# Optimization experiments

Measured on AMD Instinct MI355X. Metric: run time of the kernel, lower is better.

The kernel has to match this reference:

```python
import jax, jax.numpy as jnp
import numpy as np


def setup_inputs() -> dict:
    key = jax.random.key(0)
    k1, k2 = jax.random.split(key)
    B, S, D, E = 8, 8192, 512, 209
    x = jax.random.normal(k1, (B, S, D), dtype=jnp.float32)
    # nn.init.normal_(std=0.01)
    gate_w = jax.random.normal(k2, (E, D), dtype=jnp.float32) * 0.01
    expert_counts = jnp.zeros((E,), dtype=jnp.float32)
    gate_probs_sum = jnp.zeros((E,), dtype=jnp.float32)
    return {"x": x, "gate_w": gate_w, "expert_counts": expert_counts,
            "gate_probs_sum": gate_probs_sum}


def reference(x, gate_w, expert_counts, gate_probs_sum):
    B, S, D = x.shape
    E = gate_w.shape[0]
    x_flat = x.reshape(-1, D)                      # [N, D]
    n_tokens = x_flat.shape[0]
    gate_logits = jnp.einsum('nd,ed->ne', x_flat, gate_w)   # [N, E]
    gate_probs = jax.nn.softmax(gate_logits, axis=-1)
    gate_scores = jnp.max(gate_probs, axis=-1)               # [N]
    expert_indices = jnp.argmax(gate_probs, axis=-1)         # [N] int
    # one-hot sum over tokens == histogram of expert assignments
    tokens_per_expert_actual = jnp.zeros((E,), dtype=jnp.float32).at[expert_indices].add(1.0)
    gate_mean = jnp.mean(gate_probs, axis=0)                 # [E]
    load_balancing_loss = E * jnp.sum(gate_mean * tokens_per_expert_actual) / n_tokens
    # EMA buffer updates (no-grad in the original)
    new_expert_counts = 0.9 * expert_counts + 0.1 * tokens_per_expert_actual
    new_gate_probs_sum = 0.9 * gate_probs_sum + 0.1 * jnp.sum(gate_probs, axis=0)
    return (x_flat, gate_scores, expert_indices, load_balancing_loss,
            new_expert_counts, new_gate_probs_sum)
```

## Files before the change

kernel.cpp:

```cpp
#include <hip/hip_runtime.h>

#define DK 512
#define NSTEP 16
#define NPANEL 14
#define EPAD 224
#define LP 225
#define WFRAG_ELEMS (EPAD * DK)
#define STEPB 14336

typedef __attribute__((ext_vector_type(8))) short bf16x8;
typedef __attribute__((ext_vector_type(4))) float f32x4;

__device__ __forceinline__ unsigned short f2b(float f) {
    unsigned u = __float_as_uint(f);
    return (unsigned short)((u + 0x7fffu + ((u >> 16) & 1u)) >> 16);
}
__device__ __forceinline__ float b2f(unsigned short h) {
    return __uint_as_float((unsigned)h << 16);
}
__device__ __forceinline__ void split4(float4 v, ushort4& h, ushort4& lo) {
    h.x = f2b(v.x); h.y = f2b(v.y); h.z = f2b(v.z); h.w = f2b(v.w);
    lo.x = f2b(v.x - b2f(h.x)); lo.y = f2b(v.y - b2f(h.y));
    lo.z = f2b(v.z - b2f(h.z)); lo.w = f2b(v.w - b2f(h.w));
}
__device__ __forceinline__ void pack8(float4 a, float4 b, bf16x8& h, bf16x8& lo) {
    float v[8] = {a.x, a.y, a.z, a.w, b.x, b.y, b.z, b.w};
    #pragma unroll
    for (int j = 0; j < 8; ++j) {
        unsigned u = __float_as_uint(v[j]);
        h[j]  = (short)(u >> 16);
        lo[j] = (short)f2b(v[j] - __uint_as_float(u & 0xffff0000u));
    }
}
__device__ __forceinline__ void gld16(const void* g, void* l) {
    __builtin_amdgcn_global_load_lds(
        (const __attribute__((address_space(1))) unsigned int*)g,
        (__attribute__((address_space(3))) unsigned int*)l, 16, 0, 0);
}

extern "C" __global__ void moe_init(float* hist, float* probsum, int* cnt) {
    int t = threadIdx.x;
    if (t < EPAD) { hist[t] = 0.f; probsum[t] = 0.f; }
    if (t == 0) *cnt = 0;
}

extern "C" __global__ void __launch_bounds__(256)
moe_prep(const float* __restrict__ w,
         unsigned short* __restrict__ wHi,
         unsigned short* __restrict__ wLo, int E)
{
    int g = blockIdx.x * 256 + threadIdx.x;
    int l  = g & 63;
    int pc = g >> 6;
    int kk = pc / NPANEL;
    int p  = pc - kk * NPANEL;
    int e  = p * 16 + (l & 15);
    int k0 = kk * 32 + (l >> 4) * 8;
    float4 v0 = make_float4(0.f,0.f,0.f,0.f), v1 = v0;
    if (e < E) {
        v0 = *(const float4*)(w + (size_t)e * DK + k0);
        v1 = *(const float4*)(w + (size_t)e * DK + k0 + 4);
    }
    ushort4 h0, l0, h1, l1;
    split4(v0, h0, l0); split4(v1, h1, l1);
    size_t off = (size_t)g * 8;
    *(ushort4*)(wHi + off)     = h0;
    *(ushort4*)(wHi + off + 4) = h1;
    *(ushort4*)(wLo + off)     = l0;
    *(ushort4*)(wLo + off + 4) = l1;
}

extern "C" __global__ void __launch_bounds__(256, 2)
moe_gemm(const float* __restrict__ x,
         const unsigned short* __restrict__ wHi,
         const unsigned short* __restrict__ wLo,
         float* __restrict__ out,
         float* __restrict__ hist,
         float* __restrict__ probsum_g,
         int* __restrict__ flag_cnt,
         int* __restrict__ flag_list,
         int flag_cap, int N, int E)
{
    __shared__ char Bl[2][2 * STEPB];
    __shared__ float ps_l[EPAD];
    __shared__ float tok_m[32], tok_s[32];

    const int t    = threadIdx.x;
    const int l    = t & 63;
    const int wid  = t >> 6;
    const int wm   = wid >> 1;
    const int wn   = wid & 1;
    const int le   = l & 15;
    const int lg   = l >> 4;
    const int tok0 = blockIdx.x * 64;

    if (t < EPAD) ps_l[t] = 0.f;

    f32x4 acc[2][7];
    #pragma unroll
    for (int mi = 0; mi < 2; ++mi)
        #pragma unroll
        for (int j = 0; j < 7; ++j)
            acc[mi][j] = (f32x4){0.f, 0.f, 0.f, 0.f};

    #define STAGE_B(kk_, buf_)                                                  \
        {   _Pragma("unroll")                                                   \
            for (int i_ = 0; i_ < 7; ++i_) {                                    \
                int c_ = wid * 7 + i_;                                          \
                const char* src_ = (c_ < NPANEL)                                \
                    ? ((const char*)wHi + (kk_) * STEPB + c_ * 1024 + l * 16)   \
                    : ((const char*)wLo + (kk_) * STEPB + (c_ - NPANEL) * 1024 + l * 16); \
                gld16(src_, (buf_) + c_ * 1024);                                \
            }                                                                   \
        }

    float4 Areg[2][2][2];
    #pragma unroll
    for (int mi = 0; mi < 2; ++mi) {
        const float* ar = x + (size_t)(tok0 + wm * 32 + mi * 16 + le) * DK + lg * 8;
        Areg[0][mi][0] = *(const float4*)(ar);
        Areg[0][mi][1] = *(const float4*)(ar + 4);
    }
    STAGE_B(0, Bl[0]);
    __syncthreads();

    #pragma unroll
    for (int kk = 0; kk < NSTEP; ++kk) {
        const int p = kk & 1;
        if (kk + 1 < NSTEP) {
            #pragma unroll
            for (int mi = 0; mi < 2; ++mi) {
                const float* ar = x + (size_t)(tok0 + wm * 32 + mi * 16 + le) * DK
                                + (kk + 1) * 32 + lg * 8;
                Areg[1 - p][mi][0] = *(const float4*)(ar);
                Areg[1 - p][mi][1] = *(const float4*)(ar + 4);
            }
            STAGE_B(kk + 1, Bl[1 - p]);
        }
        if (wn == 0) {
            #pragma unroll
            for (int mi = 0; mi < 2; ++mi) {
                float* ow = out + (size_t)(tok0 + wm * 32 + mi * 16 + le) * DK
                          + kk * 32 + lg * 8;
                *(float4*)ow       = Areg[p][mi][0];
                *(float4*)(ow + 4) = Areg[p][mi][1];
            }
        }
        bf16x8 ah[2], al[2];
        pack8(Areg[p][0][0], Areg[p][0][1], ah[0], al[0]);
        pack8(Areg[p][1][0], Areg[p][1][1], ah[1], al[1]);
        #pragma unroll
        for (int j = 0; j < 7; ++j) {
            int q = wn * 7 + j;
            bf16x8 bh = *(const bf16x8*)(&Bl[p][q * 1024 + l * 16]);
            bf16x8 bl = *(const bf16x8*)(&Bl[p][STEPB + q * 1024 + l * 16]);
            #pragma unroll
            for (int mi = 0; mi < 2; ++mi) {
                acc[mi][j] = __builtin_amdgcn_mfma_f32_16x16x32_bf16(ah[mi], bh, acc[mi][j], 0, 0, 0);
                acc[mi][j] = __builtin_amdgcn_mfma_f32_16x16x32_bf16(ah[mi], bl, acc[mi][j], 0, 0, 0);
                acc[mi][j] = __builtin_amdgcn_mfma_f32_16x16x32_bf16(al[mi], bh, acc[mi][j], 0, 0, 0);
            }
        }
        __syncthreads();
    }

    float* logits = (float*)&Bl[0][0];

    for (int pass = 0; pass < 2; ++pass) {
        __syncthreads();
        if (wm == pass) {
            #pragma unroll
            for (int mi = 0; mi < 2; ++mi)
                #pragma unroll
                for (int nj = 0; nj < 7; ++nj)
                    #pragma unroll
                    for (int rg = 0; rg < 4; ++rg) {
                        int rr = mi * 16 + (l >> 4) * 4 + rg;
                        int cc = wn * 112 + nj * 16 + (l & 15);
                        logits[rr * LP + cc] = acc[mi][nj][rg];
                    }
        }
        __syncthreads();
        {
            int r = t >> 3, sub = t & 7;
            float m1 = -1e30f, m2 = -1e30f;
            int i1 = 0x7fffffff;
            for (int e = sub; e < E; e += 8) {
                float v = logits[r * LP + e];
                if (v > m1) { m2 = m1; m1 = v; i1 = e; }
                else if (v > m2) { m2 = v; }
            }
            #pragma unroll
            for (int mask = 1; mask < 8; mask <<= 1) {
                float om1 = __shfl_xor(m1, mask);
                float om2 = __shfl_xor(m2, mask);
                int   oi1 = __shfl_xor(i1, mask);
                if (om1 > m1 || (om1 == m1 && oi1 < i1)) {
                    m2 = fmaxf(m1, om2); m1 = om1; i1 = oi1;
                } else {
                    m2 = fmaxf(m2, om1);
                }
            }
            float s = 0.f;
            for (int e = sub; e < E; e += 8) s += __expf(logits[r * LP + e] - m1);
            #pragma unroll
            for (int mask = 1; mask < 8; mask <<= 1) s += __shfl_xor(s, mask);

            if (sub == 0) {
                float sinv = 1.0f / s;
                tok_m[r] = m1; tok_s[r] = sinv;
                int tok = tok0 + pass * 32 + r;
                out[(size_t)N * DK + tok]     = sinv;
                out[(size_t)N * DK + N + tok] = (float)i1;
                atomicAdd(&hist[i1], 1.0f);
                if (m1 - m2 < 2e-4f) {
                    int pos = atomicAdd(flag_cnt, 1);
                    if (pos < flag_cap) flag_list[pos] = tok;
                }
            }
        }
        __syncthreads();
        if (t < E) {
            float sum = 0.f;
            #pragma unroll 4
            for (int r = 0; r < 32; ++r)
                sum += __expf(logits[r * LP + t] - tok_m[r]) * tok_s[r];
            ps_l[t] += sum;
        }
    }
    __syncthreads();
    if (t < E) atomicAdd(&probsum_g[t], ps_l[t]);
    #undef STAGE_B
}

extern "C" __global__ void __launch_bounds__(256)
moe_refine(const float* __restrict__ x,
           const float* __restrict__ w,
           float* __restrict__ hist,
           const int* __restrict__ flag_cnt,
           const int* __restrict__ flag_list,
           int flag_cap,
           float* __restrict__ out,
           int N, int E)
{
    __shared__ float  xsh[DK];
    __shared__ double rv[256];
    __shared__ int    ri[256];
    int nf = *flag_cnt; if (nf > flag_cap) nf = flag_cap;
    const int tid = threadIdx.x;

    for (int li = blockIdx.x; li < nf; li += gridDim.x) {
        int tok = flag_list[li];
        for (int k = tid; k < DK; k += 256) xsh[k] = x[(size_t)tok * DK + k];
        __syncthreads();
        double a = -1e300;
        if (tid < E) {
            const float* wr = w + (size_t)tid * DK;
            double a0 = 0, a1 = 0, a2 = 0, a3 = 0;
            for (int k = 0; k < DK; k += 4) {
                a0 += (double)xsh[k]     * (double)wr[k];
                a1 += (double)xsh[k + 1] * (double)wr[k + 1];
                a2 += (double)xsh[k + 2] * (double)wr[k + 2];
                a3 += (double)xsh[k + 3] * (double)wr[k + 3];
            }
            a = (a0 + a1) + (a2 + a3);
        }
        rv[tid] = a; ri[tid] = tid;
        __syncthreads();
        for (int s = 128; s > 0; s >>= 1) {
            if (tid < s) {
                double vb = rv[tid + s]; int ib = ri[tid + s];
                double va = rv[tid];     int ia = ri[tid];
                if (vb > va || (vb == va && ib < ia)) { rv[tid] = vb; ri[tid] = ib; }
            }
            __syncthreads();
        }
        if (tid == 0) {
            int newi = ri[0];
            int oldi = (int)out[(size_t)N * DK + N + tok];
            if (newi != oldi) {
                atomicAdd(&hist[oldi], -1.0f);
                atomicAdd(&hist[newi],  1.0f);
                out[(size_t)N * DK + N + tok] = (float)newi;
            }
        }
        __syncthreads();
    }
}

extern "C" __global__ void __launch_bounds__(256)
moe_final(const float* __restrict__ hist,
          const float* __restrict__ probsum,
          const float* __restrict__ ec_in,
          const float* __restrict__ gps_in,
          float* __restrict__ out,
          int N, int E)
{
    __shared__ double red[256];
    int t = threadIdx.x;
    double p = 0.0;
    if (t < E) p = (double)hist[t] * (double)probsum[t];
    red[t] = p;
    __syncthreads();
    for (int s = 128; s > 0; s >>= 1) {
        if (t < s) red[t] += red[t + s];
        __syncthreads();
    }
    size_t base = (size_t)N * DK + 2 * (size_t)N;
    if (t == 0) {
        double loss = (double)E * red[0] / ((double)N * (double)N);
        out[base] = (float)loss;
    }
    if (t < E) {
        out[base + 1 + t]     = 0.9f * ec_in[t]  + 0.1f * hist[t];
        out[base + 1 + E + t] = 0.9f * gps_in[t] + 0.1f * probsum[t];
    }
}

extern "C" void kernel_launch(void* const* d_in, const int* in_sizes, int n_in,
                              void* d_out, int out_size, void* d_ws, size_t ws_size,
                              hipStream_t stream)
{
    const float* x   = (const float*)d_in[0];
    const float* w   = (const float*)d_in[1];
    const float* ec  = (const float*)d_in[2];
    const float* gps = (const float*)d_in[3];
    float* out = (float*)d_out;

    int E = in_sizes[2];
    int N = in_sizes[0] / DK;

    unsigned short* wHi = (unsigned short*)d_ws;
    unsigned short* wLo = wHi + WFRAG_ELEMS;
    float* hist    = (float*)(wLo + WFRAG_ELEMS);
    float* probsum = hist + EPAD;
    int*   cnt     = (int*)(probsum + EPAD);
    int*   list    = cnt + 1;
    long long used = 2LL * WFRAG_ELEMS * 2 + 4LL * (2 * EPAD + 1);
    long long cap_ll = ((long long)ws_size - used) / 4;
    int cap = cap_ll < 0 ? 0 : (cap_ll > 65536 ? 65536 : (int)cap_ll);

    moe_prep  <<<56,     256, 0, stream>>>(w, wHi, wLo, E);
    moe_init  <<<1,      256, 0, stream>>>(hist, probsum, cnt);
    moe_gemm  <<<N / 64, 256, 0, stream>>>(x, wHi, wLo, out, hist, probsum, cnt, list, cap, N, E);
    moe_refine<<<256,    256, 0, stream>>>(x, w, hist, cnt, list, cap, out, N, E);
    moe_final <<<1,      256, 0, stream>>>(hist, probsum, ec, gps, out, N, E);
}
```

Measured before the change: 201.0 us.

## Switch gate GEMM to single fp16 MFMA, split x copy into separate kernel

```diff
diff --git a/kernel.cpp b/kernel.cpp
--- a/kernel.cpp
+++ b/kernel.cpp
@@ -5,33 +5,12 @@
 #define NPANEL 14
 #define EPAD 224
 #define LP 225
-#define WFRAG_ELEMS (EPAD * DK)
+#define WF_ELEMS (EPAD * DK)
 #define STEPB 14336
 
-typedef __attribute__((ext_vector_type(8))) short bf16x8;
+typedef __attribute__((ext_vector_type(8))) _Float16 f16x8;
 typedef __attribute__((ext_vector_type(4))) float f32x4;
 
-__device__ __forceinline__ unsigned short f2b(float f) {
-    unsigned u = __float_as_uint(f);
-    return (unsigned short)((u + 0x7fffu + ((u >> 16) & 1u)) >> 16);
-}
-__device__ __forceinline__ float b2f(unsigned short h) {
-    return __uint_as_float((unsigned)h << 16);
-}
-__device__ __forceinline__ void split4(float4 v, ushort4& h, ushort4& lo) {
-    h.x = f2b(v.x); h.y = f2b(v.y); h.z = f2b(v.z); h.w = f2b(v.w);
-    lo.x = f2b(v.x - b2f(h.x)); lo.y = f2b(v.y - b2f(h.y));
-    lo.z = f2b(v.z - b2f(h.z)); lo.w = f2b(v.w - b2f(h.w));
-}
-__device__ __forceinline__ void pack8(float4 a, float4 b, bf16x8& h, bf16x8& lo) {
-    float v[8] = {a.x, a.y, a.z, a.w, b.x, b.y, b.z, b.w};
-    #pragma unroll
-    for (int j = 0; j < 8; ++j) {
-        unsigned u = __float_as_uint(v[j]);
-        h[j]  = (short)(u >> 16);
-        lo[j] = (short)f2b(v[j] - __uint_as_float(u & 0xffff0000u));
-    }
-}
 __device__ __forceinline__ void gld16(const void* g, void* l) {
     __builtin_amdgcn_global_load_lds(
         (const __attribute__((address_space(1))) unsigned int*)g,
@@ -45,9 +24,7 @@
 }
 
 extern "C" __global__ void __launch_bounds__(256)
-moe_prep(const float* __restrict__ w,
-         unsigned short* __restrict__ wHi,
-         unsigned short* __restrict__ wLo, int E)
+moe_prep(const float* __restrict__ w, _Float16* __restrict__ wF, int E)
 {
     int g = blockIdx.x * 256 + threadIdx.x;
     int l  = g & 63;
@@ -61,19 +38,25 @@
         v0 = *(const float4*)(w + (size_t)e * DK + k0);
         v1 = *(const float4*)(w + (size_t)e * DK + k0 + 4);
     }
-    ushort4 h0, l0, h1, l1;
-    split4(v0, h0, l0); split4(v1, h1, l1);
-    size_t off = (size_t)g * 8;
-    *(ushort4*)(wHi + off)     = h0;
-    *(ushort4*)(wHi + off + 4) = h1;
-    *(ushort4*)(wLo + off)     = l0;
-    *(ushort4*)(wLo + off + 4) = l1;
-}
-
-extern "C" __global__ void __launch_bounds__(256, 2)
+    f16x8 h;
+    h[0] = (_Float16)v0.x; h[1] = (_Float16)v0.y;
+    h[2] = (_Float16)v0.z; h[3] = (_Float16)v0.w;
+    h[4] = (_Float16)v1.x; h[5] = (_Float16)v1.y;
+    h[6] = (_Float16)v1.z; h[7] = (_Float16)v1.w;
+    *(f16x8*)(wF + (size_t)g * 8) = h;
+}
+
+extern "C" __global__ void __launch_bounds__(256)
+moe_copy(const float4* __restrict__ xin, float4* __restrict__ outv, int n4)
+{
+    int i = blockIdx.x * 256 + threadIdx.x;
+    int stride = gridDim.x * 256;
+    for (; i < n4; i += stride) outv[i] = xin[i];
+}
+
+extern "C" __global__ void __launch_bounds__(256, 4)
 moe_gemm(const float* __restrict__ x,
-         const unsigned short* __restrict__ wHi,
-         const unsigned short* __restrict__ wLo,
+         const _Float16* __restrict__ wF,
          float* __restrict__ out,
          float* __restrict__ hist,
          float* __restrict__ probsum_g,
@@ -81,9 +64,11 @@
          int* __restrict__ flag_list,
          int flag_cap, int N, int E)
 {
-    __shared__ char Bl[2][2 * STEPB];
+    __shared__ float sbuf[32 * LP];
     __shared__ float ps_l[EPAD];
     __shared__ float tok_m[32], tok_s[32];
+    char* Bl0 = (char*)sbuf;
+    char* Bl1 = (char*)sbuf + STEPB;
 
     const int t    = threadIdx.x;
     const int l    = t & 63;
@@ -93,6 +78,7 @@
     const int le   = l & 15;
     const int lg   = l >> 4;
     const int tok0 = blockIdx.x * 64;
+    const char* wFb = (const char*)wF;
 
     if (t < EPAD) ps_l[t] = 0.f;
 
@@ -103,68 +89,72 @@
         for (int j = 0; j < 7; ++j)
             acc[mi][j] = (f32x4){0.f, 0.f, 0.f, 0.f};
 
+    float4 A0[2][2], A1[2][2];
+
     #define STAGE_B(kk_, buf_)                                                  \
         {   _Pragma("unroll")                                                   \
-            for (int i_ = 0; i_ < 7; ++i_) {                                    \
-                int c_ = wid * 7 + i_;                                          \
-                const char* src_ = (c_ < NPANEL)                                \
-                    ? ((const char*)wHi + (kk_) * STEPB + c_ * 1024 + l * 16)   \
-                    : ((const char*)wLo + (kk_) * STEPB + (c_ - NPANEL) * 1024 + l * 16); \
-                gld16(src_, (buf_) + c_ * 1024);                                \
+            for (int i_ = 0; i_ < 4; ++i_) {                                    \
+                int c_ = wid * 4 + i_;                                          \
+                if (c_ < NPANEL)                                                \
+                    gld16(wFb + (size_t)(kk_) * STEPB + c_ * 1024 + l * 16,     \
+                          (buf_) + c_ * 1024);                                  \
             }                                                                   \
         }
-
-    float4 Areg[2][2][2];
-    #pragma unroll
-    for (int mi = 0; mi < 2; ++mi) {
-        const float* ar = x + (size_t)(tok0 + wm * 32 + mi * 16 + le) * DK + lg * 8;
-        Areg[0][mi][0] = *(const float4*)(ar);
-        Areg[0][mi][1] = *(const float4*)(ar + 4);
-    }
-    STAGE_B(0, Bl[0]);
+    #define LOAD_A(dst_, kk_)                                                   \
+        {   _Pragma("unroll")                                                   \
+            for (int mi_ = 0; mi_ < 2; ++mi_) {                                 \
+                const float* ar_ = x + (size_t)(tok0 + wm * 32 + mi_ * 16 + le) * DK \
+                                 + (kk_) * 32 + lg * 8;                         \
+                dst_[mi_][0] = *(const float4*)ar_;                             \
+                dst_[mi_][1] = *(const float4*)(ar_ + 4);                       \
+            }                                                                   \
+        }
+    #define COMPUTE(Asrc_, Bbase_)                                              \
+        {   f16x8 af_[2];                                                       \
+            _Pragma("unroll")                                                   \
+            for (int mi_ = 0; mi_ < 2; ++mi_) {                                 \
+                float vv_[8] = {Asrc_[mi_][0].x, Asrc_[mi_][0].y,               \
+                                Asrc_[mi_][0].z, Asrc_[mi_][0].w,               \
+                                Asrc_[mi_][1].x, Asrc_[mi_][1].y,               \
+                                Asrc_[mi_][1].z, Asrc_[mi_][1].w};              \
+                _Pragma("unroll")                                               \
+                for (int j_ = 0; j_ < 8; ++j_) af_[mi_][j_] = (_Float16)vv_[j_]; \
+            }                                                                   \
+            _Pragma("unroll")                                                   \
+            for (int j_ = 0; j_ < 7; ++j_) {                                    \
+                int q_ = wn * 7 + j_;                                           \
+                f16x8 bf_ = *(const f16x8*)((Bbase_) + q_ * 1024 + l * 16);     \
+                _Pragma("unroll")                                               \
+                for (int mi_ = 0; mi_ < 2; ++mi_)                               \
+                    acc[mi_][j_] = __builtin_amdgcn_mfma_f32_16x16x32_f16(      \
+                        af_[mi_], bf_, acc[mi_][j_], 0, 0, 0);                  \
+            }                                                                   \
+        }
+
+    LOAD_A(A0, 0);
+    STAGE_B(0, Bl0);
     __syncthreads();
 
-    #pragma unroll
-    for (int kk = 0; kk < NSTEP; ++kk) {
-        const int p = kk & 1;
-        if (kk + 1 < NSTEP) {
-            #pragma unroll
-            for (int mi = 0; mi < 2; ++mi) {
-                const float* ar = x + (size_t)(tok0 + wm * 32 + mi * 16 + le) * DK
-                                + (kk + 1) * 32 + lg * 8;
-                Areg[1 - p][mi][0] = *(const float4*)(ar);
-                Areg[1 - p][mi][1] = *(const float4*)(ar + 4);
-            }
-            STAGE_B(kk + 1, Bl[1 - p]);
-        }
-        if (wn == 0) {
-            #pragma unroll
-            for (int mi = 0; mi < 2; ++mi) {
-                float* ow = out + (size_t)(tok0 + wm * 32 + mi * 16 + le) * DK
-                          + kk * 32 + lg * 8;
-                *(float4*)ow       = Areg[p][mi][0];
-                *(float4*)(ow + 4) = Areg[p][mi][1];
-            }
-        }
-        bf16x8 ah[2], al[2];
-        pack8(Areg[p][0][0], Areg[p][0][1], ah[0], al[0]);
-        pack8(Areg[p][1][0], Areg[p][1][1], ah[1], al[1]);
-        #pragma unroll
-        for (int j = 0; j < 7; ++j) {
-            int q = wn * 7 + j;
-            bf16x8 bh = *(const bf16x8*)(&Bl[p][q * 1024 + l * 16]);
-            bf16x8 bl = *(const bf16x8*)(&Bl[p][STEPB + q * 1024 + l * 16]);
-            #pragma unroll
-            for (int mi = 0; mi < 2; ++mi) {
-                acc[mi][j] = __builtin_amdgcn_mfma_f32_16x16x32_bf16(ah[mi], bh, acc[mi][j], 0, 0, 0);
-                acc[mi][j] = __builtin_amdgcn_mfma_f32_16x16x32_bf16(ah[mi], bl, acc[mi][j], 0, 0, 0);
-                acc[mi][j] = __builtin_amdgcn_mfma_f32_16x16x32_bf16(al[mi], bh, acc[mi][j], 0, 0, 0);
-            }
-        }
-        __syncthreads();
-    }
-
-    float* logits = (float*)&Bl[0][0];
+    #pragma unroll 1
+    for (int kb = 0; kb < NSTEP / 2; ++kb) {
+        const int e = 2 * kb;
+        LOAD_A(A1, e + 1);
+        STAGE_B(e + 1, Bl1);
+        COMPUTE(A0, Bl0);
+        __syncthreads();
+        const int o = e + 1;
+        if (o + 1 < NSTEP) {
+            LOAD_A(A0, o + 1);
+            STAGE_B(o + 1, Bl0);
+        }
+        COMPUTE(A1, Bl1);
+        __syncthreads();
+    }
+    #undef LOAD_A
+    #undef COMPUTE
+    #undef STAGE_B
+
+    float* logits = sbuf;
 
     for (int pass = 0; pass < 2; ++pass) {
         __syncthreads();
@@ -213,7 +203,7 @@
                 out[(size_t)N * DK + tok]     = sinv;
                 out[(size_t)N * DK + N + tok] = (float)i1;
                 atomicAdd(&hist[i1], 1.0f);
-                if (m1 - m2 < 2e-4f) {
+                if (m1 - m2 < 1e-3f) {
                     int pos = atomicAdd(flag_cnt, 1);
                     if (pos < flag_cap) flag_list[pos] = tok;
                 }
@@ -230,7 +220,6 @@
     }
     __syncthreads();
     if (t < E) atomicAdd(&probsum_g[t], ps_l[t]);
-    #undef STAGE_B
 }
 
 extern "C" __global__ void __launch_bounds__(256)
@@ -330,19 +319,21 @@
     int E = in_sizes[2];
     int N = in_sizes[0] / DK;
 
-    unsigned short* wHi = (unsigned short*)d_ws;
-    unsigned short* wLo = wHi + WFRAG_ELEMS;
-    float* hist    = (float*)(wLo + WFRAG_ELEMS);
+    _Float16* wF   = (_Float16*)d_ws;
+    float* hist    = (float*)(wF + WF_ELEMS);
     float* probsum = hist + EPAD;
     int*   cnt     = (int*)(probsum + EPAD);
     int*   list    = cnt + 1;
-    long long used = 2LL * WFRAG_ELEMS * 2 + 4LL * (2 * EPAD + 1);
+    long long used = 2LL * WF_ELEMS + 4LL * (2 * EPAD + 1);
     long long cap_ll = ((long long)ws_size - used) / 4;
     int cap = cap_ll < 0 ? 0 : (cap_ll > 65536 ? 65536 : (int)cap_ll);
 
-    moe_prep  <<<56,     256, 0, stream>>>(w, wHi, wLo, E);
+    int n4 = (N * DK) / 4;
+
+    moe_prep  <<<56,     256, 0, stream>>>(w, wF, E);
     moe_init  <<<1,      256, 0, stream>>>(hist, probsum, cnt);
-    moe_gemm  <<<N / 64, 256, 0, stream>>>(x, wHi, wLo, out, hist, probsum, cnt, list, cap, N, E);
+    moe_gemm  <<<N / 64, 256, 0, stream>>>(x, wF, out, hist, probsum, cnt, list, cap, N, E);
+    moe_copy  <<<2048,   256, 0, stream>>>((const float4*)x, (float4*)out, n4);
     moe_refine<<<256,    256, 0, stream>>>(x, w, hist, cnt, list, cap, out, N, E);
     moe_final <<<1,      256, 0, stream>>>(hist, probsum, ec, gps, out, N, E);
 }
```

After: 245.9 us. +22.3%, slower.
